# Kernel tuning notes

Hardware: AMD Instinct MI355X
Metric: run time of the kernel (lower is better)

The kernel has to match this reference:

```python
import jax, jax.numpy as jnp
import numpy as np
import math

D_MODEL = 256
D_STATE = 16
D_CONV = 4
EXPAND = 2
N_HEADS = 4
D_INNER = EXPAND * D_MODEL          # 512
DT_RANK = (D_MODEL + 15) // 16      # 16
B_SZ, SEQ = 4, 2048


def setup_inputs() -> dict:
    key = jax.random.key(0)
    ks = jax.random.split(key, 12)
    rn = lambda i, shp, sc=0.02: jax.random.normal(ks[i], shp, dtype=jnp.float32) * sc
    x = jax.random.normal(ks[0], (B_SZ, SEQ, D_MODEL), dtype=jnp.float32)
    return dict(
        x=x,
        ln_g=jnp.ones((D_MODEL,), jnp.float32),
        ln_b=jnp.zeros((D_MODEL,), jnp.float32),
        W_in=rn(1, (D_MODEL, 2 * D_INNER)),
        conv_w=rn(2, (D_INNER, D_CONV), 0.1),
        conv_b=jnp.zeros((D_INNER,), jnp.float32),
        W_xproj=rn(3, (D_INNER, DT_RANK + 2 * D_STATE)),
        W_dt=rn(4, (DT_RANK, D_INNER), 0.1),
        b_dt=jnp.full((D_INNER,), -4.6, jnp.float32),  # softplus ~ 0.01 init
        A_log=jnp.log(jnp.tile(jnp.arange(1, D_STATE + 1, dtype=jnp.float32), (D_INNER, 1))),
        Dp=jnp.ones((D_INNER,), jnp.float32),
        W_out_m=rn(5, (D_INNER, D_MODEL)),
        W_qkv=rn(6, (D_MODEL, 3 * D_MODEL)),
        b_qkv=jnp.zeros((3 * D_MODEL,), jnp.float32),
        W_o=rn(7, (D_MODEL, D_MODEL)),
        b_o=jnp.zeros((D_MODEL,), jnp.float32),
        W_gate=rn(8, (2 * D_MODEL, D_MODEL)),
        b_gate=jnp.zeros((D_MODEL,), jnp.float32),
    )


def _sssd_forward(x, ln_g, ln_b, W_in, conv_w, conv_b, W_xproj, W_dt, b_dt,
                  A_log, Dp, W_out_m, W_qkv, b_qkv, W_o, b_o, W_gate, b_gate):
    B, L, D = x.shape
    # LayerNorm
    mu = x.mean(-1, keepdims=True)
    var = x.var(-1, keepdims=True)
    xn = (x - mu) * jax.lax.rsqrt(var + 1e-5) * ln_g + ln_b

    # ---- Mamba branch ----
    xz = xn @ W_in                      # (B,L,2*D_INNER)
    xm, z = jnp.split(xz, 2, axis=-1)
    # causal depthwise conv1d (kernel D_CONV)
    xp = jnp.pad(xm, ((0, 0), (D_CONV - 1, 0), (0, 0)))
    xc = conv_b + sum(xp[:, k:k + L, :] * conv_w[:, k] for k in range(D_CONV))
    xc = jax.nn.silu(xc)
    dbl = xc @ W_xproj                  # (B,L,DT_RANK+2*D_STATE)
    dt_in = dbl[..., :DT_RANK]
    Bm = dbl[..., DT_RANK:DT_RANK + D_STATE]
    Cm = dbl[..., DT_RANK + D_STATE:]
    dt = jax.nn.softplus(dt_in @ W_dt + b_dt)   # (B,L,D_INNER)
    A = -jnp.exp(A_log)                 # (D_INNER, D_STATE)

    def step(h, inp):
        x_t, dt_t, B_t, C_t = inp       # (B,Din),(B,Din),(B,N),(B,N)
        dA = jnp.exp(dt_t[..., None] * A)               # (B,Din,N)
        h = dA * h + (dt_t * x_t)[..., None] * B_t[:, None, :]
        y = jnp.einsum('bdn,bn->bd', h, C_t)
        return h, y

    h0 = jnp.zeros((B, D_INNER, D_STATE), x.dtype)
    xs = (jnp.swapaxes(xc, 0, 1), jnp.swapaxes(dt, 0, 1),
          jnp.swapaxes(Bm, 0, 1), jnp.swapaxes(Cm, 0, 1))
    _, ys = jax.lax.scan(step, h0, xs)
    y = jnp.swapaxes(ys, 0, 1) + xc * Dp
    y = y * jax.nn.silu(z)
    ssm_out = y @ W_out_m               # (B,L,D)

    # ---- MHSA branch (eval: no dropout) ----
    hd = D // N_HEADS
    qkv = xn @ W_qkv + b_qkv
    q, k, v = jnp.split(qkv, 3, axis=-1)
    sh = lambda t: t.reshape(B, L, N_HEADS, hd).transpose(0, 2, 1, 3)
    q, k, v = sh(q), sh(k), sh(v)
    scores = jnp.einsum('bhqd,bhkd->bhqk', q, k) * (1.0 / math.sqrt(hd))
    attn = jax.nn.softmax(scores, axis=-1)
    o = jnp.einsum('bhqk,bhkd->bhqd', attn, v).transpose(0, 2, 1, 3).reshape(B, L, D)
    attn_out = o @ W_o + b_o

    # ---- sigmoid gate fusion ----
    gate = jax.nn.sigmoid(jnp.concatenate([ssm_out, attn_out], axis=-1) @ W_gate + b_gate)
    fused = gate * ssm_out + (1.0 - gate) * attn_out
    return x + fused


def reference(x, ln_g, ln_b, W_in, conv_w, conv_b, W_xproj, W_dt, b_dt,
              A_log, Dp, W_out_m, W_qkv, b_qkv, W_o, b_o, W_gate, b_gate):
    return _sssd_forward(x, ln_g, ln_b, W_in, conv_w, conv_b, W_xproj, W_dt, b_dt,
                         A_log, Dp, W_out_m, W_qkv, b_qkv, W_o, b_o, W_gate, b_gate)
```

## Files before the change

### kernel.cpp

```cpp
#include <hip/hip_runtime.h>
#include <math.h>

#define B_SZ 4
#define SEQ 2048
#define DM 256
#define DI 512
#define DS 16
#define DTR 16
#define NH 4
#define HD 64
#define T_TOK (B_SZ*SEQ)
#define NCH 64
#define CL (SEQ/NCH)
#define QSCALE 0.18033688f

typedef short bf16x8 __attribute__((ext_vector_type(8)));
typedef float f32x4  __attribute__((ext_vector_type(4)));
typedef float f32x16 __attribute__((ext_vector_type(16)));
typedef unsigned short u16;

__device__ __forceinline__ float sigmoidf_(float x){ return 1.f/(1.f+__expf(-x)); }
__device__ __forceinline__ u16 f2bf(float x){
  unsigned int u = __float_as_uint(x);
  u += 0x7fffu + ((u>>16)&1u);
  return (u16)(u>>16);
}
__device__ __forceinline__ float bf2f(u16 u){ return __uint_as_float(((unsigned)u)<<16); }
__device__ __forceinline__ unsigned cvt_pk_bf16(float lo, float hi){
  unsigned r;
  asm("v_cvt_pk_bf16_f32 %0, %1, %2" : "=v"(r) : "v"(lo), "v"(hi));
  return r;
}

struct TcvtArgs {
  const float* src[6];
  u16* dst[6];
  int K[6];
  int Nvalid[6];
  int Npad[6];
};
__global__ __launch_bounds__(256) void tcvt_all(TcvtArgs a) {
  int wi = blockIdx.z;
  int K = a.K[wi], Nv = a.Nvalid[wi], Np = a.Npad[wi];
  int k0 = blockIdx.x*64, n0 = blockIdx.y*64;
  if (k0 >= K || n0 >= Np) return;
  __shared__ u16 tile[64][65];
  const float* src = a.src[wi];
  u16* dst = a.dst[wi];
  int tn = threadIdx.x & 63, tq = threadIdx.x >> 6;
#pragma unroll
  for (int j=0;j<16;++j){
    int kk = j*4 + tq;
    int n = n0 + tn;
    tile[tn][kk] = (n < Nv) ? f2bf(src[(size_t)(k0+kk)*Nv + n]) : (u16)0;
  }
  __syncthreads();
#pragma unroll
  for (int j=0;j<16;++j){
    int nn = j*4 + tq;
    dst[(size_t)(n0+nn)*K + k0 + tn] = tile[nn][tn];
  }
}

__global__ __launch_bounds__(256) void ln_kernel(const float* __restrict__ x,
    const float* __restrict__ g, const float* __restrict__ b,
    u16* __restrict__ xn_bf) {
  int wid = threadIdx.x >> 6;
  int lane = threadIdx.x & 63;
  int token = blockIdx.x*4 + wid;
  const float* xr = x + (size_t)token*DM;
  float4 v = *(const float4*)&xr[lane*4];
  float s  = v.x+v.y+v.z+v.w;
  float ss = v.x*v.x+v.y*v.y+v.z*v.z+v.w*v.w;
  for (int m=1;m<64;m<<=1){ s += __shfl_xor(s,m); ss += __shfl_xor(ss,m); }
  float mu  = s * (1.f/DM);
  float var = ss*(1.f/DM) - mu*mu;
  float rs  = rsqrtf(var + 1e-5f);
  float4 gv = *(const float4*)&g[lane*4];
  float4 bv = *(const float4*)&b[lane*4];
  uint2 o;
  o.x = cvt_pk_bf16((v.x-mu)*rs*gv.x + bv.x, (v.y-mu)*rs*gv.y + bv.y);
  o.y = cvt_pk_bf16((v.z-mu)*rs*gv.z + bv.z, (v.w-mu)*rs*gv.w + bv.w);
  *(uint2*)&xn_bf[(size_t)token*DM + lane*4] = o;
}

template<int ACT>
__global__ __launch_bounds__(256) void gemm_mfma(const u16* __restrict__ A,
    const u16* __restrict__ Wt, const float* __restrict__ bias,
    float* __restrict__ C, u16* __restrict__ Cbf, int K, int ldc, int nvalid,
    int qcols, float qscale, const float* __restrict__ xres,
    const float* __restrict__ cat2, u16* __restrict__ vTout) {
  __shared__ u16 lds[12288];
  int tid = threadIdx.x;
  int m0 = blockIdx.y*128, n0 = blockIdx.x*64;
  int w = tid>>6, l = tid&63, lq = l&15, lg = l>>4;
  int wm = w>>1, wn = w&1;
  f32x4 acc[4][2] = {};
  for (int k0 = 0; k0 < K; k0 += 64) {
#pragma unroll
    for (int i=0;i<4;++i){
      int gid = i*256 + tid;
      int row = gid>>3, g = gid&7;
      *(bf16x8*)&lds[row*64 + ((g ^ (row&7))*8)] =
          *(const bf16x8*)&A[(size_t)(m0+row)*K + k0 + g*8];
    }
#pragma unroll
    for (int i=0;i<2;++i){
      int gid = i*256 + tid;
      int row = gid>>3, g = gid&7;
      *(bf16x8*)&lds[8192 + row*64 + ((g ^ (row&7))*8)] =
          *(const bf16x8*)&Wt[(size_t)(n0+row)*K + k0 + g*8];
    }
    __syncthreads();
#pragma unroll
    for (int ks=0;ks<2;++ks){
      bf16x8 af[4], bfv[2];
#pragma unroll
      for (int mi=0;mi<4;++mi){
        int row = wm*64 + mi*16 + lq;
        af[mi] = *(bf16x8*)&lds[row*64 + (((ks*4+lg) ^ (row&7))*8)];
      }
#pragma unroll
      for (int nj=0;nj<2;++nj){
        int row = wn*32 + nj*16 + lq;
        bfv[nj] = *(bf16x8*)&lds[8192 + row*64 + (((ks*4+lg) ^ (row&7))*8)];
      }
#pragma unroll
      for (int mi=0;mi<4;++mi)
#pragma unroll
        for (int nj=0;nj<2;++nj)
          acc[mi][nj] = __builtin_amdgcn_mfma_f32_16x16x32_bf16(af[mi], bfv[nj], acc[mi][nj], 0,0,0);
    }
    __syncthreads();
  }
#pragma unroll
  for (int mi=0;mi<4;++mi){
#pragma unroll
    for (int nj=0;nj<2;++nj){
#pragma unroll
      for (int r=0;r<4;++r){
        int row = m0 + wm*64 + mi*16 + lg*4 + r;
        int col = n0 + wn*32 + nj*16 + lq;
        if (col < nvalid) {
          float v = acc[mi][nj][r];
          if (bias) v += bias[col];
          if (col < qcols) v *= qscale;
          if (ACT==2) {
            float g = sigmoidf_(v);
            float sv = cat2[(size_t)row*512 + col];
            float av = cat2[(size_t)row*512 + 256 + col];
            C[(size_t)row*256 + col] = xres[(size_t)row*256 + col] + g*sv + (1.f-g)*av;
          } else if (ACT==3) {
            Cbf[(size_t)row*ldc + col] = f2bf(v);
            if (col >= 512) {
              int bb = row>>11, ll = row&2047;
              int hh = (col-512)>>6, dd = (col-512)&63;
              vTout[(((size_t)(bb*4+hh))*64 + dd)*SEQ + ll] = f2bf(v);
            }
          } else {
            if (ACT==1) v = sigmoidf_(v);
            if (C)   C[(size_t)row*ldc + col] = v;
            if (Cbf) Cbf[(size_t)row*ldc + col] = f2bf(v);
          }
        }
      }
    }
  }
}

__global__ __launch_bounds__(256) void conv_kernel(const u16* __restrict__ xzb,
    const float* __restrict__ cw, const float* __restrict__ cb,
    u16* __restrict__ xc_bf) {
  int idx = blockIdx.x*256 + threadIdx.x;
  int d2 = (idx & 255)*2;
  int t = idx >> 8;
  int l = t & (SEQ-1);
  float acc0 = cb[d2], acc1 = cb[d2+1];
  float4 wA = *(const float4*)&cw[d2*4];
  float4 wB = *(const float4*)&cw[d2*4+4];
  const u16* base = xzb + (size_t)t*1024 + d2;
  ushort2 v;
  if (l>=3){ v = *(const ushort2*)&base[-3*1024]; acc0 += bf2f(v.x)*wA.x; acc1 += bf2f(v.y)*wB.x; }
  if (l>=2){ v = *(const ushort2*)&base[-2*1024]; acc0 += bf2f(v.x)*wA.y; acc1 += bf2f(v.y)*wB.y; }
  if (l>=1){ v = *(const ushort2*)&base[-1*1024]; acc0 += bf2f(v.x)*wA.z; acc1 += bf2f(v.y)*wB.z; }
  v = *(const ushort2*)&base[0];
  acc0 += bf2f(v.x)*wA.w; acc1 += bf2f(v.y)*wB.w;
  float r0 = acc0 * sigmoidf_(acc0);
  float r1 = acc1 * sigmoidf_(acc1);
  *(unsigned*)&xc_bf[(size_t)t*DI + d2] = cvt_pk_bf16(r0, r1);
}

__global__ __launch_bounds__(256) void dt_kernel(const float* __restrict__ dbl,
    const float* __restrict__ Wdt, const float* __restrict__ bdt,
    u16* __restrict__ dt) {
  __shared__ float sdbl[4][16];
  int wid = threadIdx.x>>6, lane = threadIdx.x&63;
  int token = blockIdx.x*4 + wid;
  if (lane < 16) sdbl[wid][lane] = dbl[(size_t)token*48 + lane];
  __syncthreads();
  float din[16];
#pragma unroll
  for (int k=0;k<16;++k) din[k] = sdbl[wid][k];
#pragma unroll
  for (int r=0;r<8;++r){
    int d = lane + r*64;
    float acc = bdt[d];
#pragma unroll
    for (int k=0;k<16;++k) acc += din[k]*Wdt[k*DI+d];
    float sp = (acc > 20.f) ? acc : log1pf(__expf(acc));
    dt[(size_t)token*DI+d] = f2bf(sp);
  }
}

__global__ __launch_bounds__(512) void scan_p1(const u16* __restrict__ xc_bf,
    const u16* __restrict__ dt, const float* __restrict__ dbl,
    const float* __restrict__ A_log, float* __restrict__ Pws, float* __restrict__ Hws) {
  __shared__ float sB[CL][16];
  int d = threadIdx.x;
  int bc = blockIdx.x;
  int b = bc >> 6, c = bc & 63;
  {
    int t = threadIdx.x >> 4, n = threadIdx.x & 15;
    sB[t][n] = dbl[((size_t)b*SEQ + c*CL + t)*48 + DTR + n];
  }
  __syncthreads();
  float An[16];
#pragma unroll
  for (int i=0;i<4;++i){
    float4 a = *(const float4*)&A_log[d*16 + i*4];
    An[i*4+0] = -__expf(a.x); An[i*4+1] = -__expf(a.y);
    An[i*4+2] = -__expf(a.z); An[i*4+3] = -__expf(a.w);
  }
  float h[16] = {};
  float P[16];
#pragma unroll
  for (int n=0;n<16;++n) P[n] = 1.f;
  size_t tok = (size_t)b*SEQ + c*CL;
  for (int t=0;t<CL;++t,++tok){
    float dtv = bf2f(dt[tok*DI+d]);
    float xcv = bf2f(xc_bf[tok*DI+d]);
    float u = dtv*xcv;
    float4 B0 = *(float4*)&sB[t][0];
    float4 B1 = *(float4*)&sB[t][4];
    float4 B2 = *(float4*)&sB[t][8];
    float4 B3 = *(float4*)&sB[t][12];
    float Bv[16] = {B0.x,B0.y,B0.z,B0.w,B1.x,B1.y,B1.z,B1.w,
                    B2.x,B2.y,B2.z,B2.w,B3.x,B3.y,B3.z,B3.w};
#pragma unroll
    for (int n=0;n<16;++n){
      float e = __expf(dtv*An[n]);
      P[n] *= e;
      h[n] = e*h[n] + u*Bv[n];
    }
  }
  size_t base = (((size_t)b*NCH + c)*DI + d)*16;
#pragma unroll
  for (int n=0;n<16;++n){ Pws[base+n] = P[n]; Hws[base+n] = h[n]; }
}

__global__ __launch_bounds__(256) void scan_combine(const float* __restrict__ Pws,
    const float* __restrict__ Hws, float* __restrict__ H0ws) {
  int gid = blockIdx.x*256 + threadIdx.x;
  int b  = gid >> 13;
  int dn = gid & 8191;
  float h0 = 0.f;
#pragma unroll 4
  for (int c=0;c<NCH;++c){
    size_t idx = ((size_t)(b*NCH+c)<<13) + dn;
    H0ws[idx] = h0;
    h0 = Pws[idx]*h0 + Hws[idx];
  }
}

__global__ __launch_bounds__(512) void scan_p2(const u16* __restrict__ xc_bf,
    const u16* __restrict__ dt, const float* __restrict__ dbl,
    const float* __restrict__ A_log, const float* __restrict__ Dp,
    const u16* __restrict__ xzb, const float* __restrict__ H0ws,
    u16* __restrict__ ygate_bf) {
  __shared__ float sBC[CL][32];
  int d = threadIdx.x;
  int bc = blockIdx.x;
  int b = bc >> 6, c = bc & 63;
#pragma unroll
  for (int i=0;i<2;++i){
    int idx = i*512 + threadIdx.x;
    int t = idx >> 5, q = idx & 31;
    sBC[t][q] = dbl[((size_t)b*SEQ + c*CL + t)*48 + DTR + q];
  }
  __syncthreads();
  float An[16];
#pragma unroll
  for (int i=0;i<4;++i){
    float4 a = *(const float4*)&A_log[d*16 + i*4];
    An[i*4+0] = -__expf(a.x); An[i*4+1] = -__expf(a.y);
    An[i*4+2] = -__expf(a.z); An[i*4+3] = -__expf(a.w);
  }
  float Dd = Dp[d];
  float h[16];
  size_t base = (((size_t)b*NCH + c)*DI + d)*16;
#pragma unroll
  for (int i=0;i<4;++i){
    float4 h4 = *(const float4*)&H0ws[base + i*4];
    h[i*4+0]=h4.x; h[i*4+1]=h4.y; h[i*4+2]=h4.z; h[i*4+3]=h4.w;
  }
  size_t tok = (size_t)b*SEQ + c*CL;
  for (int t=0;t<CL;++t,++tok){
    float dtv = bf2f(dt[tok*DI+d]);
    float xcv = bf2f(xc_bf[tok*DI+d]);
    float zv  = bf2f(xzb[tok*1024 + DI + d]);
    float u = dtv*xcv;
    float4 B0 = *(float4*)&sBC[t][0];
    float4 B1 = *(float4*)&sBC[t][4];
    float4 B2 = *(float4*)&sBC[t][8];
    float4 B3 = *(float4*)&sBC[t][12];
    float4 C0 = *(float4*)&sBC[t][16];
    float4 C1 = *(float4*)&sBC[t][20];
    float4 C2 = *(float4*)&sBC[t][24];
    float4 C3 = *(float4*)&sBC[t][28];
    float Bv[16] = {B0.x,B0.y,B0.z,B0.w,B1.x,B1.y,B1.z,B1.w,
                    B2.x,B2.y,B2.z,B2.w,B3.x,B3.y,B3.z,B3.w};
    float Cv[16] = {C0.x,C0.y,C0.z,C0.w,C1.x,C1.y,C1.z,C1.w,
                    C2.x,C2.y,C2.z,C2.w,C3.x,C3.y,C3.z,C3.w};
    float y = 0.f;
#pragma unroll
    for (int n=0;n<16;++n){
      float e = __expf(dtv*An[n]);
      h[n] = e*h[n] + u*Bv[n];
      y += h[n]*Cv[n];
    }
    y += xcv*Dd;
    ygate_bf[tok*DI + d] = f2bf(y * (zv*sigmoidf_(zv)));
  }
}

__global__ __launch_bounds__(256) void attn_mfma_kernel(const u16* __restrict__ qkvb,
    const u16* __restrict__ vT,
    float* __restrict__ Opart, float* __restrict__ ml) {
  __shared__ u16 lds[8192];
  int H = blockIdx.x + 8*blockIdx.y + 128*(int)blockIdx.z;
  int cx = H & 7, kk = H >> 3;
  int xq = kk & 7;
  int G  = cx*8 + (kk >> 3);
  int bh = G & 15, s = G >> 4;
  int b = bh>>2, h = bh&3;
  int tid = threadIdx.x;
  int w = tid>>6, l = tid&63;
  int lo32 = l & 31;
  int hi = l >> 5;
  size_t bbase = (size_t)b*SEQ;
  size_t vbase = (size_t)bh*HD*SEQ;
  int q_base = xq*256 + w*64;

  bf16x8 qf[2][4];
#pragma unroll
  for (int qg=0; qg<2; ++qg)
#pragma unroll
    for (int dsl=0; dsl<4; ++dsl)
      qf[qg][dsl] = *(const bf16x8*)&qkvb[(bbase + q_base + qg*32 + lo32)*768 + h*HD + dsl*16 + hi*8];

  float m_[2] = {-1e30f,-1e30f}, l_[2] = {0.f,0.f};
  f32x16 oacc[2][2] = {};

  int srow = tid>>3, sg = tid&7;
  int kt0 = s*8;
  bf16x8 kreg[2], vreg[2];

#define LOADT(kt) { \
  kreg[0] = *(const bf16x8*)&qkvb[(bbase + (size_t)(kt)*64 + srow)*768 + 256 + h*HD + sg*8]; \
  kreg[1] = *(const bf16x8*)&qkvb[(bbase + (size_t)(kt)*64 + srow + 32)*768 + 256 + h*HD + sg*8]; \
  vreg[0] = *(const bf16x8*)&vT[vbase + (size_t)srow*SEQ + (kt)*64 + sg*8]; \
  vreg[1] = *(const bf16x8*)&vT[vbase + (size_t)(srow+32)*SEQ + (kt)*64 + sg*8]; }
#define STORET() { \
  *(bf16x8*)&lds[srow*64 + ((sg ^ (srow&7))*8)] = kreg[0]; \
  *(bf16x8*)&lds[(srow+32)*64 + ((sg ^ ((srow+32)&7))*8)] = kreg[1]; \
  *(bf16x8*)&lds[4096 + srow*64 + ((sg ^ (srow&7))*8)] = vreg[0]; \
  *(bf16x8*)&lds[4096 + (srow+32)*64 + ((sg ^ ((srow+32)&7))*8)] = vreg[1]; }
#define EXCH(X, Y, s_own, s_oth) { \
  unsigned give = (l < 32) ? (Y) : (X); \
  unsigned got = __shfl_xor(give, 32); \
  s_own = (l < 32) ? (X) : got; \
  s_oth = (l < 32) ? got : (Y); }

  LOADT(kt0);
  for (int it=0; it<8; ++it){
    __syncthreads();
    STORET();
    __syncthreads();
    if (it < 7) LOADT(kt0+it+1);

#pragma unroll
    for (int t32=0; t32<2; ++t32){
      int krow = t32*32 + lo32;
      bf16x8 kf[4];
#pragma unroll
      for (int dsl=0; dsl<4; ++dsl)
        kf[dsl] = *(bf16x8*)&lds[krow*64 + (((dsl*2 + hi) ^ (krow&7))*8)];

      bf16x8 pf[2][2];
#pragma unroll
      for (int qg=0; qg<2; ++qg){
        f32x16 sacc = {0,0,0,0,0,0,0,0,0,0,0,0,0,0,0,0};
        __builtin_amdgcn_s_setprio(1);
#pragma unroll
        for (int dsl=0; dsl<4; ++dsl)
          sacc = __builtin_amdgcn_mfma_f32_32x32x16_bf16(kf[dsl], qf[qg][dsl], sacc, 0,0,0);
        __builtin_amdgcn_s_setprio(0);

        float tm = sacc[0];
#pragma unroll
        for (int r=1;r<16;++r) tm = fmaxf(tm, sacc[r]);
        tm = fmaxf(tm, __shfl_xor(tm, 32));
        if (__any(tm - m_[qg] > 8.f)) {
          float mn = fmaxf(m_[qg], tm);
          float sc = exp2f(m_[qg] - mn);
          m_[qg] = mn;
          l_[qg] *= sc;
#pragma unroll
          for (int r=0;r<16;++r){ oacc[qg][0][r] *= sc; oacc[qg][1][r] *= sc; }
        }
        float p[16];
        float ps = 0.f;
#pragma unroll
        for (int r=0;r<16;++r){ p[r] = exp2f(sacc[r] - m_[qg]); ps += p[r]; }
        ps += __shfl_xor(ps, 32);
        l_[qg] += ps;

        unsigned A0 = cvt_pk_bf16(p[0],p[1]),  A1 = cvt_pk_bf16(p[2],p[3]);
        unsigned B0 = cvt_pk_bf16(p[4],p[5]),  B1 = cvt_pk_bf16(p[6],p[7]);
        unsigned C0 = cvt_pk_bf16(p[8],p[9]),  C1 = cvt_pk_bf16(p[10],p[11]);
        unsigned D0 = cvt_pk_bf16(p[12],p[13]),D1 = cvt_pk_bf16(p[14],p[15]);
        unsigned s0,s1,s2,s3,s4,s5,s6,s7;
        EXCH(A0,B0,s0,s2); EXCH(A1,B1,s1,s3);
        EXCH(C0,D0,s4,s6); EXCH(C1,D1,s5,s7);
        ((unsigned*)&pf[qg][0])[0]=s0; ((unsigned*)&pf[qg][0])[1]=s1;
        ((unsigned*)&pf[qg][0])[2]=s2; ((unsigned*)&pf[qg][0])[3]=s3;
        ((unsigned*)&pf[qg][1])[0]=s4; ((unsigned*)&pf[qg][1])[1]=s5;
        ((unsigned*)&pf[qg][1])[2]=s6; ((unsigned*)&pf[qg][1])[3]=s7;
      }

      __builtin_amdgcn_s_setprio(1);
#pragma unroll
      for (int dtile=0; dtile<2; ++dtile){
        int vrow = dtile*32 + lo32;
        bf16x8 vf0 = *(bf16x8*)&lds[4096 + vrow*64 + (((t32*4 + 0 + hi) ^ (vrow&7))*8)];
        bf16x8 vf1 = *(bf16x8*)&lds[4096 + vrow*64 + (((t32*4 + 2 + hi) ^ (vrow&7))*8)];
        oacc[0][dtile] = __builtin_amdgcn_mfma_f32_32x32x16_bf16(vf0, pf[0][0], oacc[0][dtile], 0,0,0);
        oacc[0][dtile] = __builtin_amdgcn_mfma_f32_32x32x16_bf16(vf1, pf[0][1], oacc[0][dtile], 0,0,0);
        oacc[1][dtile] = __builtin_amdgcn_mfma_f32_32x32x16_bf16(vf0, pf[1][0], oacc[1][dtile], 0,0,0);
        oacc[1][dtile] = __builtin_amdgcn_mfma_f32_32x32x16_bf16(vf1, pf[1][1], oacc[1][dtile], 0,0,0);
      }
      __builtin_amdgcn_s_setprio(0);
    }
  }
#undef LOADT
#undef STORET
#undef EXCH

  int sidx = bh*4 + s;
#pragma unroll
  for (int qg=0; qg<2; ++qg){
    size_t rb = ((size_t)sidx*SEQ + q_base + qg*32 + lo32)*64;
#pragma unroll
    for (int dtile=0; dtile<2; ++dtile){
#pragma unroll
      for (int rg=0; rg<4; ++rg){
        float4 v4;
        v4.x = oacc[qg][dtile][rg*4+0];
        v4.y = oacc[qg][dtile][rg*4+1];
        v4.z = oacc[qg][dtile][rg*4+2];
        v4.w = oacc[qg][dtile][rg*4+3];
        *(float4*)&Opart[rb + dtile*32 + rg*8 + 4*hi] = v4;
      }
    }
    if (l < 32){
      ml[((size_t)sidx*SEQ + q_base + qg*32 + lo32)*2    ] = m_[qg];
      ml[((size_t)sidx*SEQ + q_base + qg*32 + lo32)*2 + 1] = l_[qg];
    }
  }
}

__global__ __launch_bounds__(256) void attn_merge_kernel(const float* __restrict__ Opart,
    const float* __restrict__ ml, u16* __restrict__ attn_bf) {
  int w = threadIdx.x>>6, lane = threadIdx.x&63;
  int R = blockIdx.x*4 + w;
  int bh = R>>11, q = R&2047;
  float m[4], lv[4];
#pragma unroll
  for (int s=0;s<4;++s){
    m[s]  = ml[((size_t)(bh*4+s)*SEQ + q)*2];
    lv[s] = ml[((size_t)(bh*4+s)*SEQ + q)*2 + 1];
  }
  float ms = fmaxf(fmaxf(m[0],m[1]),fmaxf(m[2],m[3]));
  float o = 0.f, lsum = 0.f;
#pragma unroll
  for (int s=0;s<4;++s){
    float wsc = exp2f(m[s]-ms);
    lsum += wsc*lv[s];
    o += wsc*Opart[((size_t)(bh*4+s)*SEQ + q)*64 + lane];
  }
  size_t token = (size_t)(bh>>2)*SEQ + q;
  attn_bf[token*DM + (bh&3)*HD + lane] = f2bf(o/lsum);
}

extern "C" void kernel_launch(void* const* d_in, const int* in_sizes, int n_in,
                              void* d_out, int out_size, void* d_ws, size_t ws_size,
                              hipStream_t stream) {
  const float* x      = (const float*)d_in[0];
  const float* ln_g   = (const float*)d_in[1];
  const float* ln_b   = (const float*)d_in[2];
  const float* W_in   = (const float*)d_in[3];
  const float* conv_w = (const float*)d_in[4];
  const float* conv_b = (const float*)d_in[5];
  const float* W_xproj= (const float*)d_in[6];
  const float* W_dt   = (const float*)d_in[7];
  const float* b_dt   = (const float*)d_in[8];
  const float* A_log  = (const float*)d_in[9];
  const float* Dp     = (const float*)d_in[10];
  const float* W_out_m= (const float*)d_in[11];
  const float* W_qkv  = (const float*)d_in[12];
  const float* b_qkv  = (const float*)d_in[13];
  const float* W_o    = (const float*)d_in[14];
  const float* b_o    = (const float*)d_in[15];
  const float* W_gate = (const float*)d_in[16];
  const float* b_gate = (const float*)d_in[17];
  float* out = (float*)d_out;

  float* ws = (float*)d_ws;
  u16*   xn_bf   = (u16*)(ws);
  u16*   xzb     = (u16*)(ws + 1048576);
  u16*   qkv_bf  = (u16*)(ws + 9437184);
  u16*   xc_bf   = (u16*)(ws + 12582912);
  float* dblb    = ws + 16777216;
  u16*   dtb     = (u16*)(ws + 17170432);
  u16*   ygate_bf= (u16*)(ws + 21364736);
  u16*   attn_bf = (u16*)(ws + 23461888);
  float* catb    = ws + 24510464;
  u16*   catb_bf = (u16*)(ws + 28704768);
  float* gateb   = ws + 30801920;
  u16*   Wt_all  = (u16*)(ws + 32899072);
  float* Opart = ws + 1048576;
  float* mlb   = (float*)xn_bf;
  u16*   vTb   = (u16*)gateb;
  float* Pws   = catb;
  float* Hws   = catb + 2097152;
  float* H0ws  = catb + 4194304;

  u16* Wt_in   = Wt_all;
  u16* Wt_qkv  = Wt_all + 262144;
  u16* Wt_out  = Wt_all + 458752;
  u16* Wt_o    = Wt_all + 589824;
  u16* Wt_gate = Wt_all + 655360;
  u16* Wt_xp   = Wt_all + 786432;

  TcvtArgs ta;
  ta.src[0]=W_in;    ta.dst[0]=Wt_in;   ta.K[0]=256; ta.Nvalid[0]=1024; ta.Npad[0]=1024;
  ta.src[1]=W_qkv;   ta.dst[1]=Wt_qkv;  ta.K[1]=256; ta.Nvalid[1]=768;  ta.Npad[1]=768;
  ta.src[2]=W_out_m; ta.dst[2]=Wt_out;  ta.K[2]=512; ta.Nvalid[2]=256;  ta.Npad[2]=256;
  ta.src[3]=W_o;     ta.dst[3]=Wt_o;    ta.K[3]=256; ta.Nvalid[3]=256;  ta.Npad[3]=256;
  ta.src[4]=W_gate;  ta.dst[4]=Wt_gate; ta.K[4]=512; ta.Nvalid[4]=256;  ta.Npad[4]=256;
  ta.src[5]=W_xproj; ta.dst[5]=Wt_xp;   ta.K[5]=512; ta.Nvalid[5]=48;   ta.Npad[5]=64;
  tcvt_all<<<dim3(8,16,6), 256, 0, stream>>>(ta);

  ln_kernel<<<T_TOK/4, 256, 0, stream>>>(x, ln_g, ln_b, xn_bf);
  gemm_mfma<0><<<dim3(16,64), 256, 0, stream>>>(xn_bf, Wt_in, nullptr, nullptr, xzb, 256, 1024, 1024, 0, 1.f, nullptr, nullptr, nullptr);
  gemm_mfma<3><<<dim3(12,64), 256, 0, stream>>>(xn_bf, Wt_qkv, b_qkv, nullptr, qkv_bf, 256, 768, 768, 256, QSCALE, nullptr, nullptr, vTb);
  conv_kernel<<<T_TOK, 256, 0, stream>>>(xzb, conv_w, conv_b, xc_bf);
  gemm_mfma<0><<<dim3(1,64), 256, 0, stream>>>(xc_bf, Wt_xp, nullptr, dblb, nullptr, 512, 48, 48, 0, 1.f, nullptr, nullptr, nullptr);
  dt_kernel<<<T_TOK/4, 256, 0, stream>>>(dblb, W_dt, b_dt, dtb);
  scan_p1<<<B_SZ*NCH, 512, 0, stream>>>(xc_bf, dtb, dblb, A_log, Pws, Hws);
  scan_combine<<<128, 256, 0, stream>>>(Pws, Hws, H0ws);
  scan_p2<<<B_SZ*NCH, 512, 0, stream>>>(xc_bf, dtb, dblb, A_log, Dp, xzb, H0ws, ygate_bf);
  attn_mfma_kernel<<<dim3(8, 16, 4), 256, 0, stream>>>(qkv_bf, vTb, Opart, mlb);
  attn_merge_kernel<<<8192, 256, 0, stream>>>(Opart, mlb, attn_bf);
  gemm_mfma<0><<<dim3(4,64), 256, 0, stream>>>(ygate_bf, Wt_out, nullptr, catb, catb_bf, 512, 512, 256, 0, 1.f, nullptr, nullptr, nullptr);
  gemm_mfma<0><<<dim3(4,64), 256, 0, stream>>>(attn_bf, Wt_o, b_o, catb+256, catb_bf+256, 256, 512, 256, 0, 1.f, nullptr, nullptr, nullptr);
  gemm_mfma<2><<<dim3(4,64), 256, 0, stream>>>(catb_bf, Wt_gate, b_gate, out, nullptr, 512, 256, 256, 0, 1.f, x, catb, nullptr);
}
```

Before: 250.9 us.

## Store scan chunk states and attention partials in bf16, use permlane32 swap

Converts the chunked-scan intermediates (P, H, H0) and the split-K attention partial outputs from fp32 to bf16, halving the global traffic of the scan combine and attention merge steps. It also replaces the cross-half __shfl_xor(…,32) exchanges with v_permlane32_swap and drops the s_setprio hints around the MFMA blocks. The cost is reduced precision in the carried SSM state and the partial attention accumulators, which may push errors toward tolerance limits.

```diff
diff --git a/kernel.cpp b/kernel.cpp
--- a/kernel.cpp
+++ b/kernel.cpp
@@ -30,6 +30,14 @@
   unsigned r;
   asm("v_cvt_pk_bf16_f32 %0, %1, %2" : "=v"(r) : "v"(lo), "v"(hi));
   return r;
+}
+__device__ __forceinline__ void permswap(unsigned &a, unsigned &b){
+  asm volatile("v_permlane32_swap_b32 %0, %1" : "+v"(a), "+v"(b));
+}
+__device__ __forceinline__ float xor32f(float v){
+  unsigned a = __float_as_uint(v), b = a;
+  permswap(a, b);
+  return __uint_as_float(a);
 }
 
 struct TcvtArgs {
@@ -214,7 +222,7 @@
 
 __global__ __launch_bounds__(512) void scan_p1(const u16* __restrict__ xc_bf,
     const u16* __restrict__ dt, const float* __restrict__ dbl,
-    const float* __restrict__ A_log, float* __restrict__ Pws, float* __restrict__ Hws) {
+    const float* __restrict__ A_log, u16* __restrict__ Pws, u16* __restrict__ Hws) {
   __shared__ float sB[CL][16];
   int d = threadIdx.x;
   int bc = blockIdx.x;
@@ -255,11 +263,14 @@
   }
   size_t base = (((size_t)b*NCH + c)*DI + d)*16;
 #pragma unroll
-  for (int n=0;n<16;++n){ Pws[base+n] = P[n]; Hws[base+n] = h[n]; }
-}
-
-__global__ __launch_bounds__(256) void scan_combine(const float* __restrict__ Pws,
-    const float* __restrict__ Hws, float* __restrict__ H0ws) {
+  for (int i=0;i<8;++i){
+    *(unsigned*)&Pws[base + i*2] = cvt_pk_bf16(P[i*2], P[i*2+1]);
+    *(unsigned*)&Hws[base + i*2] = cvt_pk_bf16(h[i*2], h[i*2+1]);
+  }
+}
+
+__global__ __launch_bounds__(256) void scan_combine(const u16* __restrict__ Pws,
+    const u16* __restrict__ Hws, u16* __restrict__ H0ws) {
   int gid = blockIdx.x*256 + threadIdx.x;
   int b  = gid >> 13;
   int dn = gid & 8191;
@@ -267,15 +278,15 @@
 #pragma unroll 4
   for (int c=0;c<NCH;++c){
     size_t idx = ((size_t)(b*NCH+c)<<13) + dn;
-    H0ws[idx] = h0;
-    h0 = Pws[idx]*h0 + Hws[idx];
+    H0ws[idx] = f2bf(h0);
+    h0 = bf2f(Pws[idx])*h0 + bf2f(Hws[idx]);
   }
 }
 
 __global__ __launch_bounds__(512) void scan_p2(const u16* __restrict__ xc_bf,
     const u16* __restrict__ dt, const float* __restrict__ dbl,
     const float* __restrict__ A_log, const float* __restrict__ Dp,
-    const u16* __restrict__ xzb, const float* __restrict__ H0ws,
+    const u16* __restrict__ xzb, const u16* __restrict__ H0ws,
     u16* __restrict__ ygate_bf) {
   __shared__ float sBC[CL][32];
   int d = threadIdx.x;
@@ -298,10 +309,11 @@
   float Dd = Dp[d];
   float h[16];
   size_t base = (((size_t)b*NCH + c)*DI + d)*16;
-#pragma unroll
-  for (int i=0;i<4;++i){
-    float4 h4 = *(const float4*)&H0ws[base + i*4];
-    h[i*4+0]=h4.x; h[i*4+1]=h4.y; h[i*4+2]=h4.z; h[i*4+3]=h4.w;
+  {
+    bf16x8 h8a = *(const bf16x8*)&H0ws[base];
+    bf16x8 h8b = *(const bf16x8*)&H0ws[base+8];
+#pragma unroll
+    for (int n=0;n<8;++n){ h[n] = bf2f((u16)h8a[n]); h[8+n] = bf2f((u16)h8b[n]); }
   }
   size_t tok = (size_t)b*SEQ + c*CL;
   for (int t=0;t<CL;++t,++tok){
@@ -335,7 +347,7 @@
 
 __global__ __launch_bounds__(256) void attn_mfma_kernel(const u16* __restrict__ qkvb,
     const u16* __restrict__ vT,
-    float* __restrict__ Opart, float* __restrict__ ml) {
+    u16* __restrict__ Opart, float* __restrict__ ml) {
   __shared__ u16 lds[8192];
   int H = blockIdx.x + 8*blockIdx.y + 128*(int)blockIdx.z;
   int cx = H & 7, kk = H >> 3;
@@ -376,10 +388,10 @@
   *(bf16x8*)&lds[4096 + srow*64 + ((sg ^ (srow&7))*8)] = vreg[0]; \
   *(bf16x8*)&lds[4096 + (srow+32)*64 + ((sg ^ ((srow+32)&7))*8)] = vreg[1]; }
 #define EXCH(X, Y, s_own, s_oth) { \
-  unsigned give = (l < 32) ? (Y) : (X); \
-  unsigned got = __shfl_xor(give, 32); \
-  s_own = (l < 32) ? (X) : got; \
-  s_oth = (l < 32) ? got : (Y); }
+  unsigned xa = (X), yb = (Y); \
+  permswap(xa, yb); \
+  s_own = (l < 32) ? (X) : xa; \
+  s_oth = (l < 32) ? yb : (Y); }
 
   LOADT(kt0);
   for (int it=0; it<8; ++it){
@@ -400,16 +412,14 @@
 #pragma unroll
       for (int qg=0; qg<2; ++qg){
         f32x16 sacc = {0,0,0,0,0,0,0,0,0,0,0,0,0,0,0,0};
-        __builtin_amdgcn_s_setprio(1);
 #pragma unroll
         for (int dsl=0; dsl<4; ++dsl)
           sacc = __builtin_amdgcn_mfma_f32_32x32x16_bf16(kf[dsl], qf[qg][dsl], sacc, 0,0,0);
-        __builtin_amdgcn_s_setprio(0);
 
         float tm = sacc[0];
 #pragma unroll
         for (int r=1;r<16;++r) tm = fmaxf(tm, sacc[r]);
-        tm = fmaxf(tm, __shfl_xor(tm, 32));
+        tm = fmaxf(tm, xor32f(tm));
         if (__any(tm - m_[qg] > 8.f)) {
           float mn = fmaxf(m_[qg], tm);
           float sc = exp2f(m_[qg] - mn);
@@ -422,7 +432,7 @@
         float ps = 0.f;
 #pragma unroll
         for (int r=0;r<16;++r){ p[r] = exp2f(sacc[r] - m_[qg]); ps += p[r]; }
-        ps += __shfl_xor(ps, 32);
+        ps += xor32f(ps);
         l_[qg] += ps;
 
         unsigned A0 = cvt_pk_bf16(p[0],p[1]),  A1 = cvt_pk_bf16(p[2],p[3]);
@@ -438,7 +448,6 @@
         ((unsigned*)&pf[qg][1])[2]=s6; ((unsigned*)&pf[qg][1])[3]=s7;
       }
 
-      __builtin_amdgcn_s_setprio(1);
 #pragma unroll
       for (int dtile=0; dtile<2; ++dtile){
         int vrow = dtile*32 + lo32;
@@ -449,7 +458,6 @@
         oacc[1][dtile] = __builtin_amdgcn_mfma_f32_32x32x16_bf16(vf0, pf[1][0], oacc[1][dtile], 0,0,0);
         oacc[1][dtile] = __builtin_amdgcn_mfma_f32_32x32x16_bf16(vf1, pf[1][1], oacc[1][dtile], 0,0,0);
       }
-      __builtin_amdgcn_s_setprio(0);
     }
   }
 #undef LOADT
@@ -464,12 +472,10 @@
     for (int dtile=0; dtile<2; ++dtile){
 #pragma unroll
       for (int rg=0; rg<4; ++rg){
-        float4 v4;
-        v4.x = oacc[qg][dtile][rg*4+0];
-        v4.y = oacc[qg][dtile][rg*4+1];
-        v4.z = oacc[qg][dtile][rg*4+2];
-        v4.w = oacc[qg][dtile][rg*4+3];
-        *(float4*)&Opart[rb + dtile*32 + rg*8 + 4*hi] = v4;
+        uint2 pk;
+        pk.x = cvt_pk_bf16(oacc[qg][dtile][rg*4+0], oacc[qg][dtile][rg*4+1]);
+        pk.y = cvt_pk_bf16(oacc[qg][dtile][rg*4+2], oacc[qg][dtile][rg*4+3]);
+        *(uint2*)&Opart[rb + dtile*32 + rg*8 + 4*hi] = pk;
       }
     }
     if (l < 32){
@@ -479,7 +485,7 @@
   }
 }
 
-__global__ __launch_bounds__(256) void attn_merge_kernel(const float* __restrict__ Opart,
+__global__ __launch_bounds__(256) void attn_merge_kernel(const u16* __restrict__ Opart,
     const float* __restrict__ ml, u16* __restrict__ attn_bf) {
   int w = threadIdx.x>>6, lane = threadIdx.x&63;
   int R = blockIdx.x*4 + w;
@@ -496,7 +502,7 @@
   for (int s=0;s<4;++s){
     float wsc = exp2f(m[s]-ms);
     lsum += wsc*lv[s];
-    o += wsc*Opart[((size_t)(bh*4+s)*SEQ + q)*64 + lane];
+    o += wsc*bf2f(Opart[((size_t)(bh*4+s)*SEQ + q)*64 + lane]);
   }
   size_t token = (size_t)(bh>>2)*SEQ + q;
   attn_bf[token*DM + (bh&3)*HD + lane] = f2bf(o/lsum);
@@ -538,12 +544,12 @@
   u16*   catb_bf = (u16*)(ws + 28704768);
   float* gateb   = ws + 30801920;
   u16*   Wt_all  = (u16*)(ws + 32899072);
-  float* Opart = ws + 1048576;
+  u16*   Opart = (u16*)(ws + 1048576);
   float* mlb   = (float*)xn_bf;
   u16*   vTb   = (u16*)gateb;
-  float* Pws   = catb;
-  float* Hws   = catb + 2097152;
-  float* H0ws  = catb + 4194304;
+  u16*   Pws   = (u16*)catb;
+  u16*   Hws   = (u16*)(catb + 1048576);
+  u16*   H0ws  = (u16*)(catb + 2097152);
 
   u16* Wt_in   = Wt_all;
   u16* Wt_qkv  = Wt_all + 262144;
```

Measured after the change: 242.6 us. 1.03x faster.
